# Kernel tuning notes

Measured on AMD Instinct MI355X. Metric: run time of the kernel, lower is better.

Reference implementation:

```python
import jax, jax.numpy as jnp
from jax import lax
import numpy as np

B, L, E, H = 4, 512, 1024, 128


def setup_inputs() -> dict:
    key = jax.random.key(0)
    k0, k1, k2, k3, k4, k5 = jax.random.split(key, 6)
    s = 1.0 / np.sqrt(E)
    return {
        "rec_emb": jax.random.normal(k0, (B, L, E), jnp.float32),
        "lig_emb": jax.random.normal(k1, (B, L, E), jnp.float32),
        "W1": jax.random.normal(k2, (E, H), jnp.float32) * s,
        "b1": jax.random.normal(k3, (H,), jnp.float32) * 0.01,
        "conv_w": jax.random.normal(k4, (1, H, 2, 2), jnp.float32) * (1.0 / np.sqrt(H * 4)),
        "conv_b": jax.random.normal(k5, (1,), jnp.float32) * 0.01,
    }


def reference(rec_emb, lig_emb, W1, b1, conv_w, conv_b):
    # shared fc: Linear -> ReLU (Dropout is identity in eval mode)
    rec_hid = jax.nn.relu(jnp.einsum("bie,eh->bih", rec_emb, W1) + b1)
    lig_hid = jax.nn.relu(jnp.einsum("bje,eh->bjh", lig_emb, W1) + b1)
    # outer-product bilinear map: bih,bjh->bijh, then tanh
    mat = jnp.tanh(rec_hid[:, :, None, :] * lig_hid[:, None, :, :])
    # permute to NCHW: (b, h, i, j)
    mat = jnp.transpose(mat, (0, 3, 1, 2))
    # Conv2d(H -> 1, kernel=2, padding=1): out spatial = L + 1
    y = lax.conv_general_dilated(
        mat, conv_w, window_strides=(1, 1), padding=[(1, 1), (1, 1)],
        dimension_numbers=("NCHW", "OIHW", "NCHW"),
    ) + conv_b[None, :, None, None]
    # MaxPool2d(kernel=2, stride=2), floor mode
    pooled = lax.reduce_window(
        y, -jnp.inf, lax.max,
        window_dimensions=(1, 1, 2, 2), window_strides=(1, 1, 2, 2),
        padding="VALID",
    )
    # global max over spatial dims -> (b, 1), sigmoid, flatten
    m = jnp.max(pooled, axis=(2, 3))
    return jax.nn.sigmoid(m).reshape(-1)
```

## Files before the change

kernel.cpp:

```cpp
#include <hip/hip_runtime.h>
#include <hip/hip_fp16.h>
#include <math.h>

#define BDIM 4
#define LDIM 512
#define EDIM 1024
#define HDIM 128
#define TILE 32
#define NT   16
#define K2   2.885390081777927f

typedef unsigned short ushort_t;
typedef __attribute__((ext_vector_type(8))) _Float16 half8;
typedef __attribute__((ext_vector_type(4))) float f32x4;

struct __align__(16) H8 { __half2 p[4]; };
union HU { H8 h; half8 v; };
struct __align__(8) US4 { ushort_t u[4]; };

__global__ __launch_bounds__(256) void gemm_direct(
    const float* __restrict__ rec, const float* __restrict__ lig,
    const float* __restrict__ W1, const float* __restrict__ b1,
    const float* __restrict__ cw, ushort_t* __restrict__ hid,
    ushort_t* __restrict__ wneg, float* __restrict__ wsumg) {
  if (blockIdx.x == 512) {
    __shared__ float wp[2][4];
    const int t = threadIdx.x;
    if (t < HDIM) {
      float4 w4 = *(const float4*)&cw[t * 4];
      _Float16 h0 = (_Float16)(-2.f * w4.x), h1 = (_Float16)(-2.f * w4.y);
      _Float16 h2 = (_Float16)(-2.f * w4.z), h3 = (_Float16)(-2.f * w4.w);
      wneg[0 * HDIM + t] = *(ushort_t*)&h0;
      wneg[1 * HDIM + t] = *(ushort_t*)&h1;
      wneg[2 * HDIM + t] = *(ushort_t*)&h2;
      wneg[3 * HDIM + t] = *(ushort_t*)&h3;
#pragma unroll
      for (int k = 4; k < 16; ++k) wneg[k * HDIM + t] = 0;
      float4 ws = w4;
#pragma unroll
      for (int off = 32; off > 0; off >>= 1) {
        ws.x += __shfl_down(ws.x, off, 64);
        ws.y += __shfl_down(ws.y, off, 64);
        ws.z += __shfl_down(ws.z, off, 64);
        ws.w += __shfl_down(ws.w, off, 64);
      }
      if ((t & 63) == 0) {
        wp[t >> 6][0] = ws.x; wp[t >> 6][1] = ws.y;
        wp[t >> 6][2] = ws.z; wp[t >> 6][3] = ws.w;
      }
    }
    __syncthreads();
    if (t < 4) wsumg[t] = wp[0][t] + wp[1][t];
    return;
  }

  const int gw = (int)blockIdx.x * 4 + (threadIdx.x >> 6);
  const int l = threadIdx.x & 63;
  const int strip = gw >> 3;
  const int nidx = gw & 7;
  const int r0 = strip * 16;
  const int m = l & 15, q = l >> 4;
  const float* arow = ((r0 < BDIM * LDIM)
                           ? rec + (size_t)r0 * EDIM
                           : lig + (size_t)(r0 - BDIM * LDIM) * EDIM) +
                      (size_t)m * EDIM + q * 8;
  const int col = nidx * 16 + m;
  const float* wcol = W1 + col;

  f32x4 acc = {0.f, 0.f, 0.f, 0.f};
  for (int blk = 0; blk < 8; ++blk) {
    float4 alo[4], ahi[4];
    float bw[4][8];
#pragma unroll
    for (int j = 0; j < 4; ++j) {
      const int k0 = (blk * 4 + j) * 32 + q * 8;
      alo[j] = *(const float4*)(arow + (blk * 4 + j) * 32);
      ahi[j] = *(const float4*)(arow + (blk * 4 + j) * 32 + 4);
#pragma unroll
      for (int kk = 0; kk < 8; ++kk)
        bw[j][kk] = wcol[(size_t)(k0 + kk) * HDIM];
    }
#pragma unroll
    for (int j = 0; j < 4; ++j) {
      HU au, bu;
      au.h.p[0] = __floats2half2_rn(alo[j].x, alo[j].y);
      au.h.p[1] = __floats2half2_rn(alo[j].z, alo[j].w);
      au.h.p[2] = __floats2half2_rn(ahi[j].x, ahi[j].y);
      au.h.p[3] = __floats2half2_rn(ahi[j].z, ahi[j].w);
      bu.h.p[0] = __floats2half2_rn(bw[j][0], bw[j][1]);
      bu.h.p[1] = __floats2half2_rn(bw[j][2], bw[j][3]);
      bu.h.p[2] = __floats2half2_rn(bw[j][4], bw[j][5]);
      bu.h.p[3] = __floats2half2_rn(bw[j][6], bw[j][7]);
      acc = __builtin_amdgcn_mfma_f32_16x16x32_f16(au.v, bu.v, acc, 0, 0, 0);
    }
  }
  const float scale = (r0 < BDIM * LDIM) ? -K2 : 1.0f;
  const float bias = b1[col];
#pragma unroll
  for (int r = 0; r < 4; ++r) {
    float v = fmaxf(acc[r] + bias, 0.f) * scale;
    ((_Float16*)hid)[(size_t)(r0 + q * 4 + r) * HDIM + col] = (_Float16)v;
  }
}

__global__ __launch_bounds__(512, 8) void bilinear_max(
    const ushort_t* __restrict__ hid, const ushort_t* __restrict__ wneg,
    const float* __restrict__ wsumg, const float* __restrict__ cw,
    const float* __restrict__ cb, float* __restrict__ partial) {
  __shared__ ushort_t rl[33][130];
  __shared__ ushort_t ll[33][130];
  __shared__ ushort_t sl4[33][34][4];
  __shared__ float wred[8];

  const int t = threadIdx.x;
  const int b = blockIdx.z;
  const int ib = (int)blockIdx.y * TILE - 1;
  const int jb = (int)blockIdx.x * TILE - 1;
  const int w = t >> 6, l = t & 63;
  const int q = l >> 4, c15 = l & 15;

  half8 wf[4];
#pragma unroll
  for (int c = 0; c < 4; ++c)
    wf[c] = *(const half8*)&wneg[c15 * HDIM + c * 32 + q * 8];
  const float wsum_v = (c15 < 4) ? wsumg[c15] : 0.f;

  H8 z;
  z.p[0] = z.p[1] = z.p[2] = z.p[3] = __floats2half2_rn(0.f, 0.f);
  for (int p = t; p < 66 * 16; p += 512) {
    int r = p >> 4, seg = (p & 15) * 8;
    if (r < 33) {
      int i = ib + r;
      H8 v = z;
      if (i >= 0) v = *(const H8*)&hid[((size_t)(b * LDIM + i)) * HDIM + seg];
      *(H8*)&rl[r][seg] = v;
    } else {
      int j = jb + (r - 33);
      H8 v = z;
      if (j >= 0) v = *(const H8*)&hid[((size_t)((BDIM + b) * LDIM + j)) * HDIM + seg];
      *(H8*)&ll[r - 33][seg] = v;
    }
  }
  __syncthreads();

  const __half2 E0 = __float2half2_rn(0.991381f);
  const __half2 E1 = __float2half2_rn(-0.818328f);
  const __half2 E2 = __float2half2_rn(0.333048f);
#define POLYG(U) __hmul2(U, __hfma2(U, __hfma2(U, E2, E1), E0))
#define GCHAIN(GU, RU, LU)                                                    \
  {                                                                           \
    __half2 u0 = h2exp2(__hmul2((RU).h.p[0], (LU).h.p[0]));                   \
    __half2 u1 = h2exp2(__hmul2((RU).h.p[1], (LU).h.p[1]));                   \
    __half2 u2 = h2exp2(__hmul2((RU).h.p[2], (LU).h.p[2]));                   \
    __half2 u3 = h2exp2(__hmul2((RU).h.p[3], (LU).h.p[3]));                   \
    (GU).h.p[0] = POLYG(u0);                                                  \
    (GU).h.p[1] = POLYG(u1);                                                  \
    (GU).h.p[2] = POLYG(u2);                                                  \
    (GU).h.p[3] = POLYG(u3);                                                  \
  }

#pragma unroll
  for (int hf = 0; hf < 2; ++hf) {
    const int jj0 = hf << 4;
    HU lu[4];
#pragma unroll
    for (int c = 0; c < 4; ++c)
      lu[c].v = *(const half8*)&ll[jj0 + c15][c * 32 + q * 8];
    const int ii = w * 4;
    f32x4 a0 = {0.f, 0.f, 0.f, 0.f}, a1 = a0, a2 = a0, a3 = a0;
#pragma unroll
    for (int c = 0; c < 4; ++c) {
      HU r0, r1, r2, r3, g0, g1, g2, g3;
      r0.v = *(const half8*)&rl[ii + 0][c * 32 + q * 8];
      r1.v = *(const half8*)&rl[ii + 1][c * 32 + q * 8];
      r2.v = *(const half8*)&rl[ii + 2][c * 32 + q * 8];
      r3.v = *(const half8*)&rl[ii + 3][c * 32 + q * 8];
      GCHAIN(g0, r0, lu[c])
      GCHAIN(g1, r1, lu[c])
      GCHAIN(g2, r2, lu[c])
      GCHAIN(g3, r3, lu[c])
      a0 = __builtin_amdgcn_mfma_f32_16x16x32_f16(g0.v, wf[c], a0, 0, 0, 0);
      a1 = __builtin_amdgcn_mfma_f32_16x16x32_f16(g1.v, wf[c], a1, 0, 0, 0);
      a2 = __builtin_amdgcn_mfma_f32_16x16x32_f16(g2.v, wf[c], a2, 0, 0, 0);
      a3 = __builtin_amdgcn_mfma_f32_16x16x32_f16(g3.v, wf[c], a3, 0, 0, 0);
    }
    if (c15 < 4) {
#pragma unroll
      for (int r = 0; r < 4; ++r) {
        _Float16 h0 = (_Float16)(wsum_v + a0[r]);
        _Float16 h1 = (_Float16)(wsum_v + a1[r]);
        _Float16 h2 = (_Float16)(wsum_v + a2[r]);
        _Float16 h3 = (_Float16)(wsum_v + a3[r]);
        sl4[ii + 0][jj0 + q * 4 + r][c15] = *(ushort_t*)&h0;
        sl4[ii + 1][jj0 + q * 4 + r][c15] = *(ushort_t*)&h1;
        sl4[ii + 2][jj0 + q * 4 + r][c15] = *(ushort_t*)&h2;
        sl4[ii + 3][jj0 + q * 4 + r][c15] = *(ushort_t*)&h3;
      }
    }
  }
#undef GCHAIN
#undef POLYG

  if (t < 260) {
    const int pr = t >> 2;
    const int o = t & 3;
    const int pi = (pr < 33) ? pr : 32;
    const int qj = (pr < 33) ? 32 : (pr - 33);
    float sa0 = 0.f, sa1 = 0.f, sa2 = 0.f, sa3 = 0.f;
    const int hb = o * 32;
    for (int h8 = hb; h8 < hb + 32; h8 += 8) {
      HU r8, l8;
      r8.v = *(const half8*)&rl[pi][h8];
      l8.v = *(const half8*)&ll[qj][h8];
#pragma unroll
      for (int j = 0; j < 4; ++j) {
        float2 pf = __half22float2(__hmul2(r8.h.p[j], l8.h.p[j]));
        float u0 = __builtin_amdgcn_exp2f(pf.x);
        float u1 = __builtin_amdgcn_exp2f(pf.y);
        float g0 = u0 * fmaf(u0, fmaf(u0, 0.333048f, -0.818328f), 0.991381f);
        float g1 = u1 * fmaf(u1, fmaf(u1, 0.333048f, -0.818328f), 0.991381f);
        float4 wa = *(const float4*)&cw[(h8 + 2 * j) * 4];
        float4 wb = *(const float4*)&cw[(h8 + 2 * j + 1) * 4];
        sa0 = fmaf(-2.f * g0, wa.x, fmaf(-2.f * g1, wb.x, sa0));
        sa1 = fmaf(-2.f * g0, wa.y, fmaf(-2.f * g1, wb.y, sa1));
        sa2 = fmaf(-2.f * g0, wa.z, fmaf(-2.f * g1, wb.z, sa2));
        sa3 = fmaf(-2.f * g0, wa.w, fmaf(-2.f * g1, wb.w, sa3));
      }
    }
    sa0 += __shfl_xor(sa0, 1, 64);
    sa1 += __shfl_xor(sa1, 1, 64);
    sa2 += __shfl_xor(sa2, 1, 64);
    sa3 += __shfl_xor(sa3, 1, 64);
    sa0 += __shfl_xor(sa0, 2, 64);
    sa1 += __shfl_xor(sa1, 2, 64);
    sa2 += __shfl_xor(sa2, 2, 64);
    sa3 += __shfl_xor(sa3, 2, 64);
    if (o == 0) {
      _Float16 h0 = (_Float16)(wsumg[0] + sa0);
      _Float16 h1 = (_Float16)(wsumg[1] + sa1);
      _Float16 h2 = (_Float16)(wsumg[2] + sa2);
      _Float16 h3 = (_Float16)(wsumg[3] + sa3);
      US4 s;
      s.u[0] = *(ushort_t*)&h0; s.u[1] = *(ushort_t*)&h1;
      s.u[2] = *(ushort_t*)&h2; s.u[3] = *(ushort_t*)&h3;
      *(US4*)&sl4[pi][qj][0] = s;
    }
  }
  __syncthreads();

  float m = -INFINITY;
  const float cbv = cb[0];
  for (int p = t; p < TILE * TILE; p += 512) {
    int jj = (p & 31) + 1, iy = (p >> 5) + 1;
    float v = cbv + (float)(*(const _Float16*)&sl4[iy - 1][jj - 1][0])
                  + (float)(*(const _Float16*)&sl4[iy - 1][jj][1])
                  + (float)(*(const _Float16*)&sl4[iy][jj - 1][2])
                  + (float)(*(const _Float16*)&sl4[iy][jj][3]);
    m = fmaxf(m, v);
  }
#pragma unroll
  for (int off = 32; off > 0; off >>= 1) m = fmaxf(m, __shfl_down(m, off, 64));
  if ((t & 63) == 0) wred[t >> 6] = m;
  __syncthreads();
  if (t == 0) {
    float mm = wred[0];
#pragma unroll
    for (int i = 1; i < 8; ++i) mm = fmaxf(mm, wred[i]);
    partial[((size_t)b * NT + blockIdx.y) * NT + blockIdx.x] = mm;
  }
}

__global__ __launch_bounds__(64) void finalize(const float* __restrict__ partial,
                                               float* __restrict__ out) {
  const int b = blockIdx.x, t = threadIdx.x;
  float m = -INFINITY;
  for (int p = t; p < NT * NT; p += 64) m = fmaxf(m, partial[b * NT * NT + p]);
#pragma unroll
  for (int off = 32; off > 0; off >>= 1) m = fmaxf(m, __shfl_down(m, off, 64));
  if (t == 0) out[b] = 1.f / (1.f + expf(-m));
}

extern "C" void kernel_launch(void* const* d_in, const int* in_sizes, int n_in,
                              void* d_out, int out_size, void* d_ws, size_t ws_size,
                              hipStream_t stream) {
  const float* rec = (const float*)d_in[0];
  const float* lig = (const float*)d_in[1];
  const float* W1  = (const float*)d_in[2];
  const float* b1  = (const float*)d_in[3];
  const float* cw  = (const float*)d_in[4];
  const float* cb  = (const float*)d_in[5];
  float* out = (float*)d_out;

  ushort_t* hid  = (ushort_t*)d_ws;
  float* partial = (float*)(hid + (size_t)2 * BDIM * LDIM * HDIM);
  ushort_t* wneg = (ushort_t*)(partial + NT * NT * BDIM);
  float* wsumg   = (float*)(wneg + 16 * HDIM);

  gemm_direct<<<dim3(513), 256, 0, stream>>>(rec, lig, W1, b1, cw, hid, wneg, wsumg);
  bilinear_max<<<dim3(NT, NT, BDIM), 512, 0, stream>>>(hid, wneg, wsumg, cw, cb, partial);
  finalize<<<dim3(BDIM), 64, 0, stream>>>(partial, out);
}
```

Before: 120.9 us.

## Stage GEMM operands in LDS with double-buffered W1 tiles

Replaces the direct-from-global projection GEMM, where each wave reloaded strided W1 columns, with a block-per-16-row version. The block converts the full 16x1024 activation strip to fp16 in shared memory and streams W1 in 128-row chunks through a double-buffered shared tile, prefetching the next chunk into registers while the MFMAs run. Each wave now computes two 16x16 output tiles. The goal is to cut redundant, uncoalesced W1 global loads. The cost is about 100KB of LDS per block, which limits occupancy, plus a syncthreads per chunk. The conv-weight setup moves into block 0, so the extra launch block is dropped.

```diff
diff --git a/kernel.cpp b/kernel.cpp
--- a/kernel.cpp
+++ b/kernel.cpp
@@ -18,14 +18,18 @@
 union HU { H8 h; half8 v; };
 struct __align__(8) US4 { ushort_t u[4]; };
 
-__global__ __launch_bounds__(256) void gemm_direct(
+__global__ __launch_bounds__(256) void gemm_lds(
     const float* __restrict__ rec, const float* __restrict__ lig,
     const float* __restrict__ W1, const float* __restrict__ b1,
     const float* __restrict__ cw, ushort_t* __restrict__ hid,
     ushort_t* __restrict__ wneg, float* __restrict__ wsumg) {
-  if (blockIdx.x == 512) {
-    __shared__ float wp[2][4];
-    const int t = threadIdx.x;
+  __shared__ ushort_t Al[16][1026];
+  __shared__ ushort_t Bl[2][128][130];
+  __shared__ float wp[2][4];
+
+  const int t = threadIdx.x;
+
+  if (blockIdx.x == 0) {
     if (t < HDIM) {
       float4 w4 = *(const float4*)&cw[t * 4];
       _Float16 h0 = (_Float16)(-2.f * w4.x), h1 = (_Float16)(-2.f * w4.y);
@@ -51,55 +55,88 @@
     }
     __syncthreads();
     if (t < 4) wsumg[t] = wp[0][t] + wp[1][t];
-    return;
-  }
-
-  const int gw = (int)blockIdx.x * 4 + (threadIdx.x >> 6);
-  const int l = threadIdx.x & 63;
-  const int strip = gw >> 3;
-  const int nidx = gw & 7;
-  const int r0 = strip * 16;
+  }
+
+  const int r0 = (int)blockIdx.x * 16;
+  const float* abase = (r0 < BDIM * LDIM)
+                           ? rec + (size_t)r0 * EDIM
+                           : lig + (size_t)(r0 - BDIM * LDIM) * EDIM;
+
+  {
+    const int sr = t >> 4, su = t & 15;
+    const float* ar = abase + (size_t)sr * EDIM;
+#pragma unroll
+    for (int p = 0; p < 16; ++p) {
+      const int c = su * 4 + p * 64;
+      f32x4 v = *(const f32x4*)(ar + c);
+      *(__half2*)&Al[sr][c] = __floats2half2_rn(v[0], v[1]);
+      *(__half2*)&Al[sr][c + 2] = __floats2half2_rn(v[2], v[3]);
+    }
+  }
+
+  const int cu4 = (t & 31) * 4, kg = t >> 5;
+  {
+#pragma unroll
+    for (int p = 0; p < 8; ++p) {
+      const int kp = p * 8 + kg;
+      f32x4 ra = *(const f32x4*)(W1 + (size_t)(2 * kp) * HDIM + cu4);
+      f32x4 rb = *(const f32x4*)(W1 + (size_t)(2 * kp + 1) * HDIM + cu4);
+#pragma unroll
+      for (int i = 0; i < 4; ++i)
+        *(__half2*)&Bl[0][cu4 + i][2 * kp] = __floats2half2_rn(ra[i], rb[i]);
+    }
+  }
+  __syncthreads();
+
+  const int w = t >> 6, l = t & 63;
   const int m = l & 15, q = l >> 4;
-  const float* arow = ((r0 < BDIM * LDIM)
-                           ? rec + (size_t)r0 * EDIM
-                           : lig + (size_t)(r0 - BDIM * LDIM) * EDIM) +
-                      (size_t)m * EDIM + q * 8;
-  const int col = nidx * 16 + m;
-  const float* wcol = W1 + col;
-
-  f32x4 acc = {0.f, 0.f, 0.f, 0.f};
-  for (int blk = 0; blk < 8; ++blk) {
-    float4 alo[4], ahi[4];
-    float bw[4][8];
-#pragma unroll
-    for (int j = 0; j < 4; ++j) {
-      const int k0 = (blk * 4 + j) * 32 + q * 8;
-      alo[j] = *(const float4*)(arow + (blk * 4 + j) * 32);
-      ahi[j] = *(const float4*)(arow + (blk * 4 + j) * 32 + 4);
-#pragma unroll
-      for (int kk = 0; kk < 8; ++kk)
-        bw[j][kk] = wcol[(size_t)(k0 + kk) * HDIM];
-    }
-#pragma unroll
-    for (int j = 0; j < 4; ++j) {
-      HU au, bu;
-      au.h.p[0] = __floats2half2_rn(alo[j].x, alo[j].y);
-      au.h.p[1] = __floats2half2_rn(alo[j].z, alo[j].w);
-      au.h.p[2] = __floats2half2_rn(ahi[j].x, ahi[j].y);
-      au.h.p[3] = __floats2half2_rn(ahi[j].z, ahi[j].w);
-      bu.h.p[0] = __floats2half2_rn(bw[j][0], bw[j][1]);
-      bu.h.p[1] = __floats2half2_rn(bw[j][2], bw[j][3]);
-      bu.h.p[2] = __floats2half2_rn(bw[j][4], bw[j][5]);
-      bu.h.p[3] = __floats2half2_rn(bw[j][6], bw[j][7]);
-      acc = __builtin_amdgcn_mfma_f32_16x16x32_f16(au.v, bu.v, acc, 0, 0, 0);
-    }
-  }
+  const int tc0 = 32 * w;
+
+  f32x4 acc0 = {0.f, 0.f, 0.f, 0.f}, acc1 = acc0;
+  for (int kc = 0; kc < 8; ++kc) {
+    const int bb = kc & 1;
+    f32x4 sa[8], sb[8];
+    if (kc < 7) {
+      const float* wb = W1 + (size_t)((kc + 1) * 128) * HDIM;
+#pragma unroll
+      for (int p = 0; p < 8; ++p) {
+        const int kp = p * 8 + kg;
+        sa[p] = *(const f32x4*)(wb + (size_t)(2 * kp) * HDIM + cu4);
+        sb[p] = *(const f32x4*)(wb + (size_t)(2 * kp + 1) * HDIM + cu4);
+      }
+    }
+#pragma unroll
+    for (int s = 0; s < 4; ++s) {
+      const int kof = s * 32 + q * 8;
+      half8 af = *(const half8*)&Al[m][kc * 128 + kof];
+      half8 b0 = *(const half8*)&Bl[bb][tc0 + m][kof];
+      half8 b1v = *(const half8*)&Bl[bb][tc0 + 16 + m][kof];
+      acc0 = __builtin_amdgcn_mfma_f32_16x16x32_f16(af, b0, acc0, 0, 0, 0);
+      acc1 = __builtin_amdgcn_mfma_f32_16x16x32_f16(af, b1v, acc1, 0, 0, 0);
+    }
+    if (kc < 7) {
+#pragma unroll
+      for (int p = 0; p < 8; ++p) {
+        const int kp = p * 8 + kg;
+#pragma unroll
+        for (int i = 0; i < 4; ++i)
+          *(__half2*)&Bl[bb ^ 1][cu4 + i][2 * kp] =
+              __floats2half2_rn(sa[p][i], sb[p][i]);
+      }
+    }
+    __syncthreads();
+  }
+
   const float scale = (r0 < BDIM * LDIM) ? -K2 : 1.0f;
-  const float bias = b1[col];
+  const float bias0 = b1[tc0 + m];
+  const float bias1 = b1[tc0 + 16 + m];
 #pragma unroll
   for (int r = 0; r < 4; ++r) {
-    float v = fmaxf(acc[r] + bias, 0.f) * scale;
-    ((_Float16*)hid)[(size_t)(r0 + q * 4 + r) * HDIM + col] = (_Float16)v;
+    const int row = r0 + q * 4 + r;
+    float v0 = fmaxf(acc0[r] + bias0, 0.f) * scale;
+    float v1 = fmaxf(acc1[r] + bias1, 0.f) * scale;
+    ((_Float16*)hid)[(size_t)row * HDIM + tc0 + m] = (_Float16)v0;
+    ((_Float16*)hid)[(size_t)row * HDIM + tc0 + 16 + m] = (_Float16)v1;
   }
 }
 
@@ -296,7 +333,7 @@
   ushort_t* wneg = (ushort_t*)(partial + NT * NT * BDIM);
   float* wsumg   = (float*)(wneg + 16 * HDIM);
 
-  gemm_direct<<<dim3(513), 256, 0, stream>>>(rec, lig, W1, b1, cw, hid, wneg, wsumg);
+  gemm_lds<<<dim3(256), 256, 0, stream>>>(rec, lig, W1, b1, cw, hid, wneg, wsumg);
   bilinear_max<<<dim3(NT, NT, BDIM), 512, 0, stream>>>(hid, wneg, wsumg, cw, cb, partial);
   finalize<<<dim3(BDIM), 64, 0, stream>>>(partial, out);
 }
```

Result: faster. 112.6 us (-6.9%).
